# Kernel tuning notes

Hardware: AMD Instinct MI355X
Metric: run time of the kernel (lower is better)

Reference implementation:

```python
import jax, jax.numpy as jnp
import numpy as np

K = 3  # kernel size


def _bilinear_sample(x, px, py):
    """Bilinear sample x:[b,c,h,w] at pixel coords px,py:[b,t,h,w].
    Zeros padding, align_corners=True semantics (coords are raw pixel coords).
    Returns [b,c,t,h,w]."""
    b, c, h, w = x.shape
    x0 = jnp.floor(px)
    y0 = jnp.floor(py)
    wx1 = px - x0
    wx0 = 1.0 - wx1
    wy1 = py - y0
    wy0 = 1.0 - wy1
    xf = x.reshape(b, c, h * w)

    def gather(xi, yi):
        valid = (xi >= 0) & (xi <= w - 1) & (yi >= 0) & (yi <= h - 1)
        xi_c = jnp.clip(xi, 0, w - 1).astype(jnp.int32)
        yi_c = jnp.clip(yi, 0, h - 1).astype(jnp.int32)
        idx = (yi_c * w + xi_c).reshape(b, 1, -1)  # [b,1,t*h*w]
        v = jnp.take_along_axis(xf, idx, axis=2).reshape(b, c, *xi.shape[1:])
        return v * valid[:, None].astype(x.dtype)

    out = (gather(x0, y0) * (wx0 * wy0)[:, None]
           + gather(x0 + 1, y0) * (wx1 * wy0)[:, None]
           + gather(x0, y0 + 1) * (wx0 * wy1)[:, None]
           + gather(x0 + 1, y0 + 1) * (wx1 * wy1)[:, None])
    return out


def setup_inputs() -> dict:
    key = jax.random.key(0)
    k1, k2, k3 = jax.random.split(key, 3)
    b, c, h, w = 4, 64, 128, 128
    out_c = 64
    x = jax.random.normal(k1, (b, c, h, w), dtype=jnp.float32)
    offset = jax.random.normal(k2, (b, 2 * K * K, h, w), dtype=jnp.float32)
    weight = jax.random.normal(k3, (out_c, c, K, K), dtype=jnp.float32) * 0.05
    bias = jnp.zeros((out_c,), dtype=jnp.float32)
    return {"x": x, "offset": offset, "weight": weight, "bias": bias}


def reference(x, offset, weight, bias):
    b, c, h, w = x.shape
    kk = K * K
    # base integer grid (x along width, y along height)
    yy, xx = jnp.meshgrid(jnp.arange(h, dtype=x.dtype), jnp.arange(w, dtype=x.dtype), indexing='ij')
    off = offset.reshape(b, kk, 2, h, w)
    # grid_sample with align_corners=True inverts the module's normalization,
    # so effective sampling coords are simply base + offset in pixel space.
    px = xx[None, None] + off[:, :, 0]  # [b,kk,h,w]
    py = yy[None, None] + off[:, :, 1]
    sampled = _bilinear_sample(x, px, py)  # [b,c,kk,h,w]
    w2 = weight.reshape(weight.shape[0], c, kk)  # [o,c,kk]
    out = jnp.einsum('oct,bcthw->bohw', w2, sampled)
    return out + bias[None, :, None, None]
```

## Files before the change

### kernel.cpp

```cpp
#include <hip/hip_runtime.h>
#include <cstddef>

#define BH 4
#define CH 64
#define OH 64
#define HH 128
#define WW 128
#define KK 9
#define HW (HH * WW)

typedef __attribute__((ext_vector_type(8))) short short8;
typedef __attribute__((ext_vector_type(4))) float f32x4;
typedef __attribute__((ext_vector_type(2))) float f32x2;
typedef __attribute__((ext_vector_type(4))) unsigned int uint4v;
typedef __attribute__((ext_vector_type(4))) unsigned short ushort4v;

__device__ __forceinline__ unsigned short f2bf(float f) {
    unsigned u = __float_as_uint(f);
    u += 0x7fffu + ((u >> 16) & 1u);
    return (unsigned short)(u >> 16);
}
__device__ __forceinline__ f32x2 bf2x2(unsigned d) {
    f32x2 r;
    r.x = __uint_as_float(d << 16);
    r.y = __uint_as_float(d & 0xffff0000u);
    return r;
}
__device__ __forceinline__ unsigned pack_bf2(f32x2 v) {
    unsigned u0 = __float_as_uint(v.x);
    u0 += 0x7fffu + ((u0 >> 16) & 1u);
    unsigned u1 = __float_as_uint(v.y);
    u1 += 0x7fffu + ((u1 >> 16) & 1u);
    return __builtin_amdgcn_perm(u1, u0, 0x07060302);
}
__device__ __forceinline__ uint4v combine4(uint4v c00, uint4v c10, uint4v c01, uint4v c11,
                                           float w00, float w10, float w01, float w11) {
    f32x2 W00 = {w00, w00}, W10 = {w10, w10}, W01 = {w01, w01}, W11 = {w11, w11};
    uint4v r;
#pragma unroll
    for (int j = 0; j < 4; ++j) {
        f32x2 s = W00 * bf2x2(c00[j]) + W10 * bf2x2(c10[j])
                + W01 * bf2x2(c01[j]) + W11 * bf2x2(c11[j]);
        r[j] = pack_bf2(s);
    }
    return r;
}

__global__ __launch_bounds__(256) void dcl_prep(const float* __restrict__ x,
                                                const float* __restrict__ wgt,
                                                unsigned short* __restrict__ xt,
                                                unsigned short* __restrict__ wtb) {
    if (blockIdx.x < 1024) {
        __shared__ float tile[64][65];
        int chunk = blockIdx.x;
        int b = chunk >> 8;
        int hw0 = (chunk & 255) * 64;
        int tid = threadIdx.x;
        int tx = tid & 63;
        int ty = tid >> 6;
        const float* xb = x + (size_t)b * CH * HW;
#pragma unroll
        for (int c = ty; c < 64; c += 4)
            tile[c][tx] = xb[(size_t)c * HW + hw0 + tx];
        __syncthreads();
        unsigned short* xtb = xt + ((size_t)b << 20);
        int c4 = (tid & 15) * 4;
        int p0 = tid >> 4;
#pragma unroll
        for (int it = 0; it < 4; ++it) {
            int pxl = p0 + it * 16;
            ushort4v v = { f2bf(tile[c4 + 0][pxl]), f2bf(tile[c4 + 1][pxl]),
                           f2bf(tile[c4 + 2][pxl]), f2bf(tile[c4 + 3][pxl]) };
            *(ushort4v*)(xtb + (size_t)(hw0 + pxl) * CH + c4) = v;
        }
    } else {
        int idx = (blockIdx.x - 1024) * 256 + threadIdx.x;
        int j  = idx & 7;
        int l  = (idx >> 3) & 63;
        int nt = (idx >> 9) & 3;
        int ks = idx >> 11;
        int k = ks * 32 + ((l >> 4) * 8) + j;
        int n = nt * 16 + (l & 15);
        int c = k & 63;
        int t = k >> 6;
        wtb[idx] = f2bf(wgt[(n * CH + c) * KK + t]);
    }
}

#define PREP_WORDS 1152
#define OAREA_WORDS 1040
#define SMEM_WORDS (2 * OAREA_WORDS)

__global__ __launch_bounds__(128, 8) void dcl_main(
        const unsigned short* __restrict__ xt,
        const float* __restrict__ offset,
        const unsigned short* __restrict__ wtb,
        const float* __restrict__ bias,
        float* __restrict__ out) {
    __shared__ int smem[SMEM_WORDS];
    int tid = threadIdx.x;
    int lane = tid & 63;
    int wave = tid >> 6;

    int P0 = blockIdx.x * 16;
    int b = P0 >> 14;
    int rem0 = P0 & (HW - 1);
    int y = rem0 >> 7;
    int x0 = rem0 & 127;
    int m = lane & 15;
    int quad = lane >> 4;

    {
#pragma unroll
        for (int rr = 0; rr < 2; ++rr) {
            int e = tid + rr * 128;
            if (e < 144) {
                int t = e >> 4;
                int pm = e & 15;
                const float* offbase = offset + (((size_t)(b * 18)) << 14) + (rem0 + pm);
                float ox = offbase[(size_t)(2 * t) << 14];
                float oy = offbase[(size_t)(2 * t + 1) << 14];
                float fx = (float)(x0 + pm) + ox;
                float fy = (float)y + oy;
                float x0f = floorf(fx), y0f = floorf(fy);
                float wx1 = fx - x0f, wy1 = fy - y0f;
                float wx0 = 1.0f - wx1, wy0 = 1.0f - wy1;
                int ix0 = (int)x0f, iy0 = (int)y0f;
                int ix1 = ix0 + 1, iy1 = iy0 + 1;
                bool vx0 = (unsigned)ix0 < (unsigned)WW;
                bool vx1 = (unsigned)ix1 < (unsigned)WW;
                bool vy0 = (unsigned)iy0 < (unsigned)HH;
                bool vy1 = (unsigned)iy1 < (unsigned)HH;
                float w00 = (vx0 && vy0) ? wx0 * wy0 : 0.0f;
                float w10 = (vx1 && vy0) ? wx1 * wy0 : 0.0f;
                float w01 = (vx0 && vy1) ? wx0 * wy1 : 0.0f;
                float w11 = (vx1 && vy1) ? wx1 * wy1 : 0.0f;
                int cx0 = min(max(ix0, 0), WW - 1), cx1 = min(max(ix1, 0), WW - 1);
                int cy0 = min(max(iy0, 0), HH - 1), cy1 = min(max(iy1, 0), HH - 1);
                int base = b << 14;
                int o00 = (base + (cy0 << 7) + cx0) << 7;
                int o10 = (base + (cy0 << 7) + cx1) << 7;
                int o01 = (base + (cy1 << 7) + cx0) << 7;
                int o11 = (base + (cy1 << 7) + cx1) << 7;
                int* pp = smem + t * 128 + pm;
                pp[0]   = __float_as_int(w00);
                pp[16]  = __float_as_int(w10);
                pp[32]  = __float_as_int(w01);
                pp[48]  = __float_as_int(w11);
                pp[64]  = o00;
                pp[80]  = o10;
                pp[96]  = o01;
                pp[112] = o11;
            }
        }
    }
    __syncthreads();

    f32x4 acc[4];
#pragma unroll
    for (int i = 0; i < 4; ++i) acc[i] = (f32x4)(0.f);

    const short8* bfrags = (const short8*)wtb;
    const char* xtb = (const char*)xt;

    int tbase = wave ? 5 : 0;
    int tcnt  = wave ? 4 : 5;
#pragma unroll
    for (int i = 0; i < 5; ++i) {
        if (i < tcnt) {
            int t = tbase + i;
            const int* pp = smem + t * 128 + m;
            float w00 = __int_as_float(pp[0]);
            float w10 = __int_as_float(pp[16]);
            float w01 = __int_as_float(pp[32]);
            float w11 = __int_as_float(pp[48]);
            int qoff = quad * 16;
            int o00 = pp[64]  + qoff;
            int o10 = pp[80]  + qoff;
            int o01 = pp[96]  + qoff;
            int o11 = pp[112] + qoff;
            uint4v c00a = *(const uint4v*)(xtb + o00);
            uint4v c10a = *(const uint4v*)(xtb + o10);
            uint4v c01a = *(const uint4v*)(xtb + o01);
            uint4v c11a = *(const uint4v*)(xtb + o11);
            uint4v c00b = *(const uint4v*)(xtb + o00 + 64);
            uint4v c10b = *(const uint4v*)(xtb + o10 + 64);
            uint4v c01b = *(const uint4v*)(xtb + o01 + 64);
            uint4v c11b = *(const uint4v*)(xtb + o11 + 64);
            uint4v ra = combine4(c00a, c10a, c01a, c11a, w00, w10, w01, w11);
            uint4v rb = combine4(c00b, c10b, c01b, c11b, w00, w10, w01, w11);
            short8 aa = __builtin_bit_cast(short8, ra);
            short8 ab = __builtin_bit_cast(short8, rb);
            int ks = 2 * t;
#pragma unroll
            for (int nt = 0; nt < 4; ++nt)
                acc[nt] = __builtin_amdgcn_mfma_f32_16x16x32_bf16(
                    aa, bfrags[(ks * 4 + nt) * 64 + lane], acc[nt], 0, 0, 0);
#pragma unroll
            for (int nt = 0; nt < 4; ++nt)
                acc[nt] = __builtin_amdgcn_mfma_f32_16x16x32_bf16(
                    ab, bfrags[((ks + 1) * 4 + nt) * 64 + lane], acc[nt], 0, 0, 0);
        }
    }

    __syncthreads();
    float* o_w = (float*)(smem + wave * OAREA_WORDS);
#pragma unroll
    for (int nt = 0; nt < 4; ++nt)
#pragma unroll
        for (int reg = 0; reg < 4; ++reg)
            o_w[(quad * 4 + reg) * 65 + nt * 16 + m] = acc[nt][reg];
    __syncthreads();

    const float* o0 = (const float*)smem;
    const float* o1 = (const float*)(smem + OAREA_WORDS);
#pragma unroll
    for (int j = tid; j < 16 * 64; j += 128) {
        int o = j >> 4;
        int p = j & 15;
        float v = o0[p * 65 + o] + o1[p * 65 + o] + bias[o];
        out[(((size_t)(b * OH + o)) << 14) + rem0 + p] = v;
    }
}

extern "C" void kernel_launch(void* const* d_in, const int* in_sizes, int n_in,
                              void* d_out, int out_size, void* d_ws, size_t ws_size,
                              hipStream_t stream) {
    const float* x      = (const float*)d_in[0];
    const float* offset = (const float*)d_in[1];
    const float* weight = (const float*)d_in[2];
    const float* bias   = (const float*)d_in[3];
    float* out = (float*)d_out;

    unsigned short* xt  = (unsigned short*)d_ws;
    unsigned short* wtb = (unsigned short*)((char*)d_ws + (size_t)BH * HW * CH * 2);

    dcl_prep<<<1024 + 144, 256, 0, stream>>>(x, weight, xt, wtb);
    dcl_main<<<(BH * HW) / 16, 128, 0, stream>>>(xt, offset, wtb, bias, out);
}
```

Measured before the change: 119.2 us.

## Process a full output row per block and stage weight fragments in LDS

```diff
diff --git a/kernel.cpp b/kernel.cpp
--- a/kernel.cpp
+++ b/kernel.cpp
@@ -87,11 +87,12 @@
     }
 }
 
-#define PREP_WORDS 1152
-#define OAREA_WORDS 1040
-#define SMEM_WORDS (2 * OAREA_WORDS)
-
-__global__ __launch_bounds__(128, 8) void dcl_main(
+#define NW 8
+#define CHUNK_BYTES 24576
+#define OSLICE_WORDS 1040
+#define SMEM_WORDS (NW * OSLICE_WORDS)
+
+__global__ __launch_bounds__(512, 4) void dcl_main(
         const unsigned short* __restrict__ xt,
         const float* __restrict__ offset,
         const unsigned short* __restrict__ wtb,
@@ -102,83 +103,69 @@
     int lane = tid & 63;
     int wave = tid >> 6;
 
-    int P0 = blockIdx.x * 16;
-    int b = P0 >> 14;
-    int rem0 = P0 & (HW - 1);
-    int y = rem0 >> 7;
-    int x0 = rem0 & 127;
+    int row = blockIdx.x;
+    int b = row >> 7;
+    int y = row & 127;
     int m = lane & 15;
     int quad = lane >> 4;
-
-    {
-#pragma unroll
-        for (int rr = 0; rr < 2; ++rr) {
-            int e = tid + rr * 128;
-            if (e < 144) {
-                int t = e >> 4;
-                int pm = e & 15;
-                const float* offbase = offset + (((size_t)(b * 18)) << 14) + (rem0 + pm);
-                float ox = offbase[(size_t)(2 * t) << 14];
-                float oy = offbase[(size_t)(2 * t + 1) << 14];
-                float fx = (float)(x0 + pm) + ox;
-                float fy = (float)y + oy;
-                float x0f = floorf(fx), y0f = floorf(fy);
-                float wx1 = fx - x0f, wy1 = fy - y0f;
-                float wx0 = 1.0f - wx1, wy0 = 1.0f - wy1;
-                int ix0 = (int)x0f, iy0 = (int)y0f;
-                int ix1 = ix0 + 1, iy1 = iy0 + 1;
-                bool vx0 = (unsigned)ix0 < (unsigned)WW;
-                bool vx1 = (unsigned)ix1 < (unsigned)WW;
-                bool vy0 = (unsigned)iy0 < (unsigned)HH;
-                bool vy1 = (unsigned)iy1 < (unsigned)HH;
-                float w00 = (vx0 && vy0) ? wx0 * wy0 : 0.0f;
-                float w10 = (vx1 && vy0) ? wx1 * wy0 : 0.0f;
-                float w01 = (vx0 && vy1) ? wx0 * wy1 : 0.0f;
-                float w11 = (vx1 && vy1) ? wx1 * wy1 : 0.0f;
-                int cx0 = min(max(ix0, 0), WW - 1), cx1 = min(max(ix1, 0), WW - 1);
-                int cy0 = min(max(iy0, 0), HH - 1), cy1 = min(max(iy1, 0), HH - 1);
-                int base = b << 14;
-                int o00 = (base + (cy0 << 7) + cx0) << 7;
-                int o10 = (base + (cy0 << 7) + cx1) << 7;
-                int o01 = (base + (cy1 << 7) + cx0) << 7;
-                int o11 = (base + (cy1 << 7) + cx1) << 7;
-                int* pp = smem + t * 128 + pm;
-                pp[0]   = __float_as_int(w00);
-                pp[16]  = __float_as_int(w10);
-                pp[32]  = __float_as_int(w01);
-                pp[48]  = __float_as_int(w11);
-                pp[64]  = o00;
-                pp[80]  = o10;
-                pp[96]  = o01;
-                pp[112] = o11;
-            }
-        }
-    }
-    __syncthreads();
+    int qoff = quad * 16;
+    int pm = wave * 16 + m;
+
+    const char* xtb = (const char*)xt;
+    const float* ob = offset + (((size_t)(b * 18)) << 14) + (y << 7) + pm;
+    float pxf = (float)pm;
+    float pyf = (float)y;
 
     f32x4 acc[4];
 #pragma unroll
     for (int i = 0; i < 4; ++i) acc[i] = (f32x4)(0.f);
 
-    const short8* bfrags = (const short8*)wtb;
-    const char* xtb = (const char*)xt;
-
-    int tbase = wave ? 5 : 0;
-    int tcnt  = wave ? 4 : 5;
-#pragma unroll
-    for (int i = 0; i < 5; ++i) {
-        if (i < tcnt) {
-            int t = tbase + i;
-            const int* pp = smem + t * 128 + m;
-            float w00 = __int_as_float(pp[0]);
-            float w10 = __int_as_float(pp[16]);
-            float w01 = __int_as_float(pp[32]);
-            float w11 = __int_as_float(pp[48]);
-            int qoff = quad * 16;
-            int o00 = pp[64]  + qoff;
-            int o10 = pp[80]  + qoff;
-            int o01 = pp[96]  + qoff;
-            int o11 = pp[112] + qoff;
+    const short8* bl = (const short8*)smem;
+
+#pragma unroll
+    for (int c = 0; c < 3; ++c) {
+        if (c) __syncthreads();
+        {
+            const uint4v* bsrc = (const uint4v*)((const char*)wtb + c * CHUNK_BYTES);
+            uint4v* bdst = (uint4v*)smem;
+#pragma unroll
+            for (int r = 0; r < 3; ++r)
+                bdst[r * 512 + tid] = bsrc[r * 512 + tid];
+        }
+        float oxv[3], oyv[3];
+#pragma unroll
+        for (int tl = 0; tl < 3; ++tl) {
+            int t = c * 3 + tl;
+            oxv[tl] = ob[(size_t)(2 * t) << 14];
+            oyv[tl] = ob[(size_t)(2 * t + 1) << 14];
+        }
+        __syncthreads();
+
+#pragma unroll
+        for (int tl = 0; tl < 3; ++tl) {
+            float fx = pxf + oxv[tl];
+            float fy = pyf + oyv[tl];
+            float x0f = floorf(fx), y0f = floorf(fy);
+            float wx1 = fx - x0f, wy1 = fy - y0f;
+            float wx0 = 1.0f - wx1, wy0 = 1.0f - wy1;
+            int ix0 = (int)x0f, iy0 = (int)y0f;
+            int ix1 = ix0 + 1, iy1 = iy0 + 1;
+            bool vx0 = (unsigned)ix0 < (unsigned)WW;
+            bool vx1 = (unsigned)ix1 < (unsigned)WW;
+            bool vy0 = (unsigned)iy0 < (unsigned)HH;
+            bool vy1 = (unsigned)iy1 < (unsigned)HH;
+            float w00 = (vx0 && vy0) ? wx0 * wy0 : 0.0f;
+            float w10 = (vx1 && vy0) ? wx1 * wy0 : 0.0f;
+            float w01 = (vx0 && vy1) ? wx0 * wy1 : 0.0f;
+            float w11 = (vx1 && vy1) ? wx1 * wy1 : 0.0f;
+            int cx0 = min(max(ix0, 0), WW - 1), cx1 = min(max(ix1, 0), WW - 1);
+            int cy0 = min(max(iy0, 0), HH - 1), cy1 = min(max(iy1, 0), HH - 1);
+            int base = b << 14;
+            int o00 = ((base + (cy0 << 7) + cx0) << 7) + qoff;
+            int o10 = ((base + (cy0 << 7) + cx1) << 7) + qoff;
+            int o01 = ((base + (cy1 << 7) + cx0) << 7) + qoff;
+            int o11 = ((base + (cy1 << 7) + cx1) << 7) + qoff;
+
             uint4v c00a = *(const uint4v*)(xtb + o00);
             uint4v c10a = *(const uint4v*)(xtb + o10);
             uint4v c01a = *(const uint4v*)(xtb + o01);
@@ -191,20 +178,21 @@
             uint4v rb = combine4(c00b, c10b, c01b, c11b, w00, w10, w01, w11);
             short8 aa = __builtin_bit_cast(short8, ra);
             short8 ab = __builtin_bit_cast(short8, rb);
-            int ks = 2 * t;
+
+            int f0 = (tl * 2) * 4;
 #pragma unroll
             for (int nt = 0; nt < 4; ++nt)
                 acc[nt] = __builtin_amdgcn_mfma_f32_16x16x32_bf16(
-                    aa, bfrags[(ks * 4 + nt) * 64 + lane], acc[nt], 0, 0, 0);
+                    aa, bl[(f0 + nt) * 64 + lane], acc[nt], 0, 0, 0);
 #pragma unroll
             for (int nt = 0; nt < 4; ++nt)
                 acc[nt] = __builtin_amdgcn_mfma_f32_16x16x32_bf16(
-                    ab, bfrags[((ks + 1) * 4 + nt) * 64 + lane], acc[nt], 0, 0, 0);
+                    ab, bl[(f0 + 4 + nt) * 64 + lane], acc[nt], 0, 0, 0);
         }
     }
 
     __syncthreads();
-    float* o_w = (float*)(smem + wave * OAREA_WORDS);
+    float* o_w = (float*)smem + wave * OSLICE_WORDS;
 #pragma unroll
     for (int nt = 0; nt < 4; ++nt)
 #pragma unroll
@@ -212,14 +200,14 @@
             o_w[(quad * 4 + reg) * 65 + nt * 16 + m] = acc[nt][reg];
     __syncthreads();
 
-    const float* o0 = (const float*)smem;
-    const float* o1 = (const float*)(smem + OAREA_WORDS);
-#pragma unroll
-    for (int j = tid; j < 16 * 64; j += 128) {
-        int o = j >> 4;
-        int p = j & 15;
-        float v = o0[p * 65 + o] + o1[p * 65 + o] + bias[o];
-        out[(((size_t)(b * OH + o)) << 14) + rem0 + p] = v;
+    const float* os = (const float*)smem;
+#pragma unroll
+    for (int j = tid; j < 64 * 128; j += 512) {
+        int o = j >> 7;
+        int p = j & 127;
+        int w2 = p >> 4, pl = p & 15;
+        float v = os[w2 * OSLICE_WORDS + pl * 65 + o] + bias[o];
+        out[(((size_t)(b * OH + o)) << 14) + (y << 7) + p] = v;
     }
 }
 
@@ -236,5 +224,5 @@
     unsigned short* wtb = (unsigned short*)((char*)d_ws + (size_t)BH * HW * CH * 2);
 
     dcl_prep<<<1024 + 144, 256, 0, stream>>>(x, weight, xt, wtb);
-    dcl_main<<<(BH * HW) / 16, 128, 0, stream>>>(xt, offset, wtb, bias, out);
-}
+    dcl_main<<<BH * HH, 512, 0, stream>>>(xt, offset, wtb, bias, out);
+}
```

Result: faster. 113.2 us (-5.0%).
